# Kernel optimization log

Measured on AMD Instinct MI355X. Metric: run time of the kernel, lower is better.

The kernel has to match this reference:

```python
import jax, jax.numpy as jnp
import numpy as np

D_MODEL = 1024
N_HEADS = 16
D_HEAD = D_MODEL // N_HEADS
D_FF = 4096
EPS = 1e-5


def layer_norm(x, g, b):
    mu = jnp.mean(x, axis=-1, keepdims=True)
    var = jnp.mean(jnp.square(x - mu), axis=-1, keepdims=True)
    return (x - mu) * jax.lax.rsqrt(var + EPS) * g + b


def setup_inputs() -> dict:
    key = jax.random.key(0)
    ks = jax.random.split(key, 8)
    s = 1.0 / np.sqrt(D_MODEL)
    return {
        "x": jax.random.normal(ks[0], (2, 2048, D_MODEL), dtype=jnp.float32),
        "Wq": jax.random.normal(ks[1], (N_HEADS, D_MODEL, D_HEAD), dtype=jnp.float32) * s,
        "Wk": jax.random.normal(ks[2], (N_HEADS, D_MODEL, D_HEAD), dtype=jnp.float32) * s,
        "Wv": jax.random.normal(ks[3], (N_HEADS, D_MODEL, D_HEAD), dtype=jnp.float32) * s,
        "Wo": jax.random.normal(ks[4], (D_MODEL, D_MODEL), dtype=jnp.float32) * s,
        "bo": jnp.zeros((D_MODEL,), dtype=jnp.float32),
        "ln1_g": jnp.ones((D_MODEL,), dtype=jnp.float32),
        "ln1_b": jnp.zeros((D_MODEL,), dtype=jnp.float32),
        "ln2_g": jnp.ones((D_MODEL,), dtype=jnp.float32),
        "ln2_b": jnp.zeros((D_MODEL,), dtype=jnp.float32),
        "W1": jax.random.normal(ks[5], (D_MODEL, D_FF), dtype=jnp.float32) * s,
        "b1": jnp.zeros((D_FF,), dtype=jnp.float32),
        "W2": jax.random.normal(ks[6], (D_FF, D_MODEL), dtype=jnp.float32) * (1.0 / np.sqrt(D_FF)),
        "b2": jnp.zeros((D_MODEL,), dtype=jnp.float32),
    }


def reference(x, Wq, Wk, Wv, Wo, bo, ln1_g, ln1_b, ln2_g, ln2_b, W1, b1, W2, b2):
    # Pre-norm MHA (per-head projections batched over head axis h)
    xn = layer_norm(x, ln1_g, ln1_b)
    q = jnp.einsum("bsd,hde->bhse", xn, Wq)
    k = jnp.einsum("bsd,hde->bhse", xn, Wk)
    v = jnp.einsum("bsd,hde->bhse", xn, Wv)
    scores = jnp.einsum("bhqe,bhke->bhqk", q, k) / jnp.sqrt(jnp.float32(D_HEAD))
    w = jax.nn.softmax(scores, axis=-1)
    attn = jnp.einsum("bhqk,bhke->bhqe", w, v)  # [b,h,s,dh]
    b, h, s, dh = attn.shape
    concat = attn.transpose(0, 2, 1, 3).reshape(b, s, h * dh)  # head concat order matches torch cat
    attn_out = concat @ Wo + bo
    hidden = x + attn_out
    hn = layer_norm(hidden, ln2_g, ln2_b)
    ff = jax.nn.gelu(hn @ W1 + b1, approximate=False) @ W2 + b2  # torch nn.GELU default = exact
    return hidden + ff
```

## Files before the change

kernel.cpp:

```cpp
#include <hip/hip_runtime.h>
#include <hip/hip_bf16.h>

typedef __bf16 bf16;
typedef __bf16 bf16x4 __attribute__((ext_vector_type(4)));
typedef __bf16 bf16x8 __attribute__((ext_vector_type(8)));
typedef float  f32x4  __attribute__((ext_vector_type(4)));

static __device__ __forceinline__ f32x4 mfma16(bf16x8 a, bf16x8 b, f32x4 c) {
  return __builtin_amdgcn_mfma_f32_16x16x32_bf16(a, b, c, 0, 0, 0);
}

static __device__ __forceinline__ float fexp2(float x) {
  return __builtin_amdgcn_exp2f(x);
}

static __device__ __forceinline__ void gl_lds16(const bf16* g, bf16* l) {
  __builtin_amdgcn_global_load_lds(
      (const __attribute__((address_space(1))) void*)g,
      (__attribute__((address_space(3))) void*)l, 16, 0, 0);
}

struct TrTab {
  const float* src[6];
  bf16* dst[6];
  int R[6], C[6], ntx[6], nty[6];
  int base[7];
};

__global__ __launch_bounds__(256) void tr6_kernel(TrTab tab) {
  int bid = blockIdx.x;
  int j = 0;
  while (j < 5 && bid >= tab.base[j + 1]) ++j;
  const int local = bid - tab.base[j];
  const int R = tab.R[j], C = tab.C[j];
  const int ntx = tab.ntx[j];
  const int per_z = ntx * tab.nty[j];
  const int z = local / per_z;
  const int rem = local - z * per_z;
  const int by = rem / ntx, bx = rem - by * ntx;
  const float* in = tab.src[j];
  bf16* out = tab.dst[j];

  __shared__ bf16 tile[32][33];
  const size_t zoff = (size_t)z * R * C;
  const int tx = threadIdx.x & 31, ty = threadIdx.x >> 5;
  const int x = bx * 32 + tx;
  const int y0 = by * 32;
#pragma unroll
  for (int jj = 0; jj < 4; ++jj)
    tile[ty + jj * 8][tx] = (bf16)in[zoff + (size_t)(y0 + ty + jj * 8) * C + x];
  __syncthreads();
  const int x2 = y0 + tx;
  const int y2 = bx * 32;
#pragma unroll
  for (int jj = 0; jj < 4; ++jj)
    out[zoff + (size_t)(y2 + ty + jj * 8) * R + x2] = tile[tx][ty + jj * 8];
}

__global__ __launch_bounds__(256) void trb_kernel(const bf16* __restrict__ inp,
                                                  bf16* __restrict__ out,
                                                  int R, int C) {
  __shared__ bf16 tile[32][33];
  const size_t zoff = (size_t)blockIdx.z * R * C;
  const int tx = threadIdx.x & 31, ty = threadIdx.x >> 5;
  const int x = blockIdx.x * 32 + tx;
  const int y0 = blockIdx.y * 32;
#pragma unroll
  for (int j = 0; j < 4; ++j)
    tile[ty + j * 8][tx] = inp[zoff + (size_t)(y0 + ty + j * 8) * C + x];
  __syncthreads();
  const int x2 = y0 + tx;
  const int y2 = blockIdx.x * 32;
#pragma unroll
  for (int j = 0; j < 4; ++j)
    out[zoff + (size_t)(y2 + ty + j * 8) * R + x2] = tile[tx][ty + j * 8];
}

__global__ __launch_bounds__(256) void ln_kernel(const float* __restrict__ inp,
                                                 const float* __restrict__ g,
                                                 const float* __restrict__ bt,
                                                 bf16* __restrict__ outp) {
  const int row = blockIdx.x;
  const int t = threadIdx.x;
  f32x4 v = ((const f32x4*)inp)[row * 256 + t];
  float s = v[0] + v[1] + v[2] + v[3];
  float sq = v[0] * v[0] + v[1] * v[1] + v[2] * v[2] + v[3] * v[3];
#pragma unroll
  for (int off = 32; off > 0; off >>= 1) {
    s += __shfl_xor(s, off);
    sq += __shfl_xor(sq, off);
  }
  __shared__ float red[8];
  const int wave = t >> 6, lane = t & 63;
  if (lane == 0) {
    red[wave] = s;
    red[wave + 4] = sq;
  }
  __syncthreads();
  s = red[0] + red[1] + red[2] + red[3];
  sq = red[4] + red[5] + red[6] + red[7];
  const float mu = s * (1.0f / 1024.0f);
  const float var = sq * (1.0f / 1024.0f) - mu * mu;
  const float rstd = rsqrtf(fmaxf(var, 0.0f) + 1e-5f);
  f32x4 gg = ((const f32x4*)g)[t];
  f32x4 bb = ((const f32x4*)bt)[t];
  bf16 o[4];
#pragma unroll
  for (int i = 0; i < 4; ++i)
    o[i] = (bf16)((v[i] - mu) * rstd * gg[i] + bb[i]);
  *(uint2*)&outp[(size_t)row * 1024 + 4 * t] = *(uint2*)o;
}

enum { EPI_QKV = 0, EPI_O = 1, EPI_FF1 = 2, EPI_FF2 = 3 };

template <int EPI, bool NARROW>
__global__ __launch_bounds__(256) void gemm_bt(
    const bf16* __restrict__ A, const bf16* __restrict__ Bt, const int K,
    const float* __restrict__ bias, const float* __restrict__ res,
    bf16* __restrict__ outB, float* __restrict__ outF) {
  constexpr int BN = NARROW ? 64 : 128;
  constexpr int NI = NARROW ? 2 : 4;
  constexpr int BCH = BN / 32;
  __shared__ __align__(16) bf16 sA[2][128 * 64];
  __shared__ __align__(16) bf16 sB[2][BN * 64];
  const int t = threadIdx.x;
  const int lane = t & 63, wave = t >> 6;
  const int quad = lane >> 4, l15 = lane & 15;
  const int wr = wave >> 1, wc = wave & 1;

  const int gx = gridDim.x;
  const int nwg = gx * gridDim.y;
  const int lin = blockIdx.y * gx + blockIdx.x;
  const int sw = (lin & 7) * (nwg >> 3) + (lin >> 3);
  const int m0 = (sw / gx) * 128, n0 = (sw % gx) * BN;

  const int srow = lane >> 3;
  const int scol = ((lane & 7) ^ srow) * 8;

  const bf16* aPtr[4];
#pragma unroll
  for (int c = 0; c < 4; ++c)
    aPtr[c] = A + (size_t)(m0 + wave * 32 + c * 8 + srow) * K + scol;
  const bf16* bPtr[BCH];
#pragma unroll
  for (int c = 0; c < BCH; ++c)
    bPtr[c] = Bt + (size_t)(n0 + wave * (BCH * 8) + c * 8 + srow) * K + scol;

  f32x4 acc[4][NI];
#pragma unroll
  for (int i = 0; i < 4; ++i)
#pragma unroll
    for (int j = 0; j < NI; ++j) acc[i][j] = {0.f, 0.f, 0.f, 0.f};

  const int niter = K >> 6;
#pragma unroll
  for (int c = 0; c < 4; ++c)
    gl_lds16(aPtr[c], &sA[0][(wave * 4 + c) * 512]);
#pragma unroll
  for (int c = 0; c < BCH; ++c)
    gl_lds16(bPtr[c], &sB[0][(wave * BCH + c) * 512]);

  for (int it = 0; it < niter; ++it) {
    const int cur = it & 1, nxt = cur ^ 1;
    __syncthreads();
    if (it + 1 < niter) {
      const int off = (it + 1) * 64;
#pragma unroll
      for (int c = 0; c < 4; ++c)
        gl_lds16(aPtr[c] + off, &sA[nxt][(wave * 4 + c) * 512]);
#pragma unroll
      for (int c = 0; c < BCH; ++c)
        gl_lds16(bPtr[c] + off, &sB[nxt][(wave * BCH + c) * 512]);
    }
#pragma unroll
    for (int ks = 0; ks < 2; ++ks) {
      bf16x8 af[4], bfr[NI];
#pragma unroll
      for (int mi = 0; mi < 4; ++mi) {
        const int row = wr * 64 + mi * 16 + l15;
        const int col = ((ks * 4 + quad) ^ (row & 7)) * 8;
        af[mi] = *(const bf16x8*)&sA[cur][row * 64 + col];
      }
#pragma unroll
      for (int ni = 0; ni < NI; ++ni) {
        const int row = wc * (BN / 2) + ni * 16 + l15;
        const int col = ((ks * 4 + quad) ^ (row & 7)) * 8;
        bfr[ni] = *(const bf16x8*)&sB[cur][row * 64 + col];
      }
#pragma unroll
      for (int mi = 0; mi < 4; ++mi)
#pragma unroll
        for (int ni = 0; ni < NI; ++ni)
          acc[mi][ni] = mfma16(af[mi], bfr[ni], acc[mi][ni]);
    }
  }

#pragma unroll
  for (int mi = 0; mi < 4; ++mi) {
#pragma unroll
    for (int ni = 0; ni < NI; ++ni) {
      const int n = n0 + wc * (BN / 2) + ni * 16 + l15;
#pragma unroll
      for (int r = 0; r < 4; ++r) {
        const int m = m0 + wr * 64 + mi * 16 + quad * 4 + r;
        float v = acc[mi][ni][r];
        if constexpr (EPI == EPI_QKV) {
          const int which = n >> 10, nn = n & 1023;
          const int h = nn >> 6, e = nn & 63;
          const int b = m >> 11, s2 = m & 2047;
          outB[(size_t)which * 4194304 +
               ((size_t)(b * 16 + h) * 2048 + s2) * 64 + e] = (bf16)v;
        } else if constexpr (EPI == EPI_O) {
          v += bias[n] + res[(size_t)m * 1024 + n];
          outF[(size_t)m * 1024 + n] = v;
        } else if constexpr (EPI == EPI_FF1) {
          v += bias[n];
          v = 0.5f * v * (1.0f + erff(v * 0.70710678118654752f));
          outB[(size_t)m * 4096 + n] = (bf16)v;
        } else {
          v += bias[n] + res[(size_t)m * 1024 + n];
          outF[(size_t)m * 1024 + n] = v;
        }
      }
    }
  }
}

__global__ __launch_bounds__(512, 4) void attn_kernel(
    const bf16* __restrict__ q, const bf16* __restrict__ k,
    const bf16* __restrict__ vt, bf16* __restrict__ ao) {
  __shared__ __align__(16) bf16 sP[256 * 72];
  __shared__ __align__(16) bf16 sK[2][64 * 64];
  __shared__ __align__(16) bf16 sV[2][64 * 64];
  const int t = threadIdx.x;
  const int lane = t & 63, wave = t >> 6;
  const int wq = wave & 3, kh = wave >> 2;
  const int quad = lane >> 4, l15 = lane & 15;

  const int lin = blockIdx.y * 16 + blockIdx.x;
  const int sw = (lin & 7) * 64 + (lin >> 3);
  const int q0 = (sw & 15) * 128;
  const int bh = sw >> 4, b = bh >> 4, h = bh & 15;

  const bf16* Q  = q  + (size_t)bh * 2048 * 64;
  const bf16* Kp = k  + (size_t)bh * 2048 * 64 + (size_t)kh * 1024 * 64;
  const bf16* Vt = vt + (size_t)bh * 64 * 2048 + kh * 1024;
  const int srow = lane >> 3;
  const int scol = ((lane & 7) ^ srow) * 8;
  const float SCL = 0.125f * 1.4426950408889634f;

#pragma unroll
  for (int c = 0; c < 2; ++c) {
    const int chunk = wave * 2 + c;
    const int row = chunk * 8 + srow;
    gl_lds16(&Q[(size_t)(q0 + row) * 64 + scol], &sP[chunk * 512]);
  }
  __syncthreads();
  bf16x8 qf[2][2];
#pragma unroll
  for (int mi = 0; mi < 2; ++mi)
#pragma unroll
    for (int ks = 0; ks < 2; ++ks) {
      const int row = wq * 32 + mi * 16 + l15;
      const int col = ((ks * 4 + quad) ^ (row & 7)) * 8;
      qf[mi][ks] = *(const bf16x8*)&sP[row * 64 + col];
    }
  __syncthreads();

  f32x4 o[2][4];
  float ls[2] = {0.f, 0.f};
#pragma unroll
  for (int mi = 0; mi < 2; ++mi)
#pragma unroll
    for (int ne = 0; ne < 4; ++ne) o[mi][ne] = {0.f, 0.f, 0.f, 0.f};

  for (int kb = 0; kb < 16; ++kb) {
    const int kbase = kb * 64;
    __syncthreads();
#pragma unroll
    for (int c = 0; c < 2; ++c) {
      const int chunk = wq * 2 + c;
      const int row = chunk * 8 + srow;
      gl_lds16(&Kp[(size_t)(kbase + row) * 64 + scol], &sK[kh][chunk * 512]);
      gl_lds16(&Vt[(size_t)row * 2048 + kbase + scol], &sV[kh][chunk * 512]);
    }
    __syncthreads();

    f32x4 s[4][2];
#pragma unroll
    for (int ni = 0; ni < 4; ++ni)
#pragma unroll
      for (int mi = 0; mi < 2; ++mi) s[ni][mi] = {0.f, 0.f, 0.f, 0.f};
#pragma unroll
    for (int ks = 0; ks < 2; ++ks) {
      bf16x8 kf[4];
#pragma unroll
      for (int ni = 0; ni < 4; ++ni) {
        const int row = ni * 16 + l15;
        const int col = ((ks * 4 + quad) ^ (row & 7)) * 8;
        kf[ni] = *(const bf16x8*)&sK[kh][row * 64 + col];
      }
#pragma unroll
      for (int ni = 0; ni < 4; ++ni)
#pragma unroll
        for (int mi = 0; mi < 2; ++mi)
          s[ni][mi] = mfma16(kf[ni], qf[mi][ks], s[ni][mi]);
    }

#pragma unroll
    for (int mi = 0; mi < 2; ++mi)
#pragma unroll
      for (int ni = 0; ni < 4; ++ni) {
        bf16x4 p4;
#pragma unroll
        for (int r = 0; r < 4; ++r) {
          const float p = fexp2(s[ni][mi][r] * SCL);
          ls[mi] += p;
          p4[r] = (bf16)p;
        }
        *(bf16x4*)&sP[(wave * 32 + mi * 16 + l15) * 72 + ni * 16 + quad * 4] =
            p4;
      }

#pragma unroll
    for (int ksb = 0; ksb < 2; ++ksb) {
      bf16x8 vf[4];
#pragma unroll
      for (int ne = 0; ne < 4; ++ne) {
        const int row = ne * 16 + l15;
        const int col = ((ksb * 4 + quad) ^ (row & 7)) * 8;
        vf[ne] = *(const bf16x8*)&sV[kh][row * 64 + col];
      }
#pragma unroll
      for (int mi = 0; mi < 2; ++mi) {
        const bf16x8 pf = *(const bf16x8*)&sP[(wave * 32 + mi * 16 + l15) * 72 +
                                              ksb * 32 + quad * 8];
#pragma unroll
        for (int ne = 0; ne < 4; ++ne)
          o[mi][ne] = mfma16(pf, vf[ne], o[mi][ne]);
      }
    }
  }

#pragma unroll
  for (int mi = 0; mi < 2; ++mi) {
    ls[mi] += __shfl_xor(ls[mi], 16);
    ls[mi] += __shfl_xor(ls[mi], 32);
  }

  float* mo = (float*)sP;
  float* ml = (float*)sK;
  __syncthreads();
  if (kh == 1) {
    const int base = (wq * 64 + lane) * 32;
#pragma unroll
    for (int mi = 0; mi < 2; ++mi)
#pragma unroll
      for (int ne = 0; ne < 4; ++ne)
        *(f32x4*)&mo[base + (mi * 4 + ne) * 4] = o[mi][ne];
    ml[(wq * 64 + lane) * 2 + 0] = ls[0];
    ml[(wq * 64 + lane) * 2 + 1] = ls[1];
  }
  __syncthreads();
  if (kh == 0) {
    const int base = (wq * 64 + lane) * 32;
#pragma unroll
    for (int mi = 0; mi < 2; ++mi) {
#pragma unroll
      for (int ne = 0; ne < 4; ++ne) {
        const f32x4 add = *(const f32x4*)&mo[base + (mi * 4 + ne) * 4];
#pragma unroll
        for (int r = 0; r < 4; ++r) o[mi][ne][r] += add[r];
      }
      ls[mi] += ml[(wq * 64 + lane) * 2 + mi];
      ls[mi] = 1.0f / fmaxf(ls[mi], 1e-30f);
    }
#pragma unroll
    for (int mi = 0; mi < 2; ++mi) {
      float linv[4];
#pragma unroll
      for (int r = 0; r < 4; ++r) linv[r] = __shfl(ls[mi], quad * 4 + r);
#pragma unroll
      for (int ne = 0; ne < 4; ++ne)
#pragma unroll
        for (int r = 0; r < 4; ++r) {
          const int row = q0 + wq * 32 + mi * 16 + quad * 4 + r;
          const int col = h * 64 + ne * 16 + l15;
          ao[((size_t)(b * 2048 + row)) * 1024 + col] =
              (bf16)(o[mi][ne][r] * linv[r]);
        }
    }
  }
}

extern "C" void kernel_launch(void* const* d_in, const int* in_sizes, int n_in,
                              void* d_out, int out_size, void* d_ws,
                              size_t ws_size, hipStream_t stream) {
  const float* x    = (const float*)d_in[0];
  const float* Wq   = (const float*)d_in[1];
  const float* Wk   = (const float*)d_in[2];
  const float* Wv   = (const float*)d_in[3];
  const float* Wo   = (const float*)d_in[4];
  const float* bo   = (const float*)d_in[5];
  const float* ln1g = (const float*)d_in[6];
  const float* ln1b = (const float*)d_in[7];
  const float* ln2g = (const float*)d_in[8];
  const float* ln2b = (const float*)d_in[9];
  const float* W1   = (const float*)d_in[10];
  const float* b1   = (const float*)d_in[11];
  const float* W2   = (const float*)d_in[12];
  const float* b2   = (const float*)d_in[13];

  char* ws = (char*)d_ws;
  const size_t MB = 1ull << 20;
  bf16* QKVT = (bf16*)(ws);
  bf16* WqT  = QKVT;
  bf16* WkT  = (bf16*)(ws + 2 * MB);
  bf16* WvT  = (bf16*)(ws + 4 * MB);
  bf16* WoT  = (bf16*)(ws + 6 * MB);
  bf16* W1T  = (bf16*)(ws + 8 * MB);
  bf16* W2T  = (bf16*)(ws + 16 * MB);
  bf16* sh8  = (bf16*)(ws + 24 * MB);
  bf16* qb   = (bf16*)(ws + 32 * MB);
  bf16* kb   = (bf16*)(ws + 40 * MB);
  bf16* vb   = (bf16*)(ws + 48 * MB);
  bf16* vtb  = (bf16*)(ws + 56 * MB);
  bf16* h1   = (bf16*)(ws + 32 * MB);
  float* hid = (float*)(ws + 64 * MB);

  const dim3 blk(256);

  TrTab tab;
  const float* srcs[6] = {Wq, Wk, Wv, Wo, W1, W2};
  bf16* dsts[6] = {WqT, WkT, WvT, WoT, W1T, W2T};
  const int Rs[6] = {1024, 1024, 1024, 1024, 1024, 4096};
  const int Cs[6] = {64, 64, 64, 1024, 4096, 1024};
  const int Zs[6] = {16, 16, 16, 1, 1, 1};
  int base = 0;
  for (int j = 0; j < 6; ++j) {
    tab.src[j] = srcs[j];
    tab.dst[j] = dsts[j];
    tab.R[j] = Rs[j];
    tab.C[j] = Cs[j];
    tab.ntx[j] = Cs[j] / 32;
    tab.nty[j] = Rs[j] / 32;
    tab.base[j] = base;
    base += (Cs[j] / 32) * (Rs[j] / 32) * Zs[j];
  }
  tab.base[6] = base;
  tr6_kernel<<<base, blk, 0, stream>>>(tab);

  ln_kernel<<<4096, blk, 0, stream>>>(x, ln1g, ln1b, sh8);
  gemm_bt<EPI_QKV, false><<<dim3(24, 32), blk, 0, stream>>>(
      sh8, QKVT, 1024, nullptr, nullptr, qb, nullptr);
  trb_kernel<<<dim3(2, 64, 32), blk, 0, stream>>>(vb, vtb, 2048, 64);
  attn_kernel<<<dim3(16, 32), dim3(512), 0, stream>>>(qb, kb, vtb, sh8);
  gemm_bt<EPI_O, false><<<dim3(8, 32), blk, 0, stream>>>(
      sh8, WoT, 1024, bo, x, nullptr, hid);
  ln_kernel<<<4096, blk, 0, stream>>>(hid, ln2g, ln2b, sh8);
  gemm_bt<EPI_FF1, false><<<dim3(32, 32), blk, 0, stream>>>(
      sh8, W1T, 1024, b1, nullptr, h1, nullptr);
  gemm_bt<EPI_FF2, true><<<dim3(16, 32), blk, 0, stream>>>(
      h1, W2T, 4096, b2, hid, nullptr, (float*)d_out);

  (void)in_sizes; (void)n_in; (void)out_size; (void)ws_size;
}
```

Measured before the change: 357.3 us.

## Single-buffer GEMM LDS tiles and add XCD-aware block remap for FF2

Removes double buffering of the A/B LDS tiles in the GEMM: each iteration now issues its global-to-LDS loads, synchronizes, computes, then synchronizes again, halving LDS use per block. This can raise occupancy, but loads no longer overlap with MFMA work from the previous tile. It also replaces the old block-index swizzle with an optional XCD-grouped row mapping, enabled only for the FF2 GEMM. The other GEMMs now use plain blockIdx ordering with no swizzle.

Measured after the change: 368.1 us. 3.0% more time.

```diff
diff --git a/kernel.cpp b/kernel.cpp
--- a/kernel.cpp
+++ b/kernel.cpp
@@ -113,7 +113,7 @@
 
 enum { EPI_QKV = 0, EPI_O = 1, EPI_FF1 = 2, EPI_FF2 = 3 };
 
-template <int EPI, bool NARROW>
+template <int EPI, bool NARROW, bool SWZ>
 __global__ __launch_bounds__(256) void gemm_bt(
     const bf16* __restrict__ A, const bf16* __restrict__ Bt, const int K,
     const float* __restrict__ bias, const float* __restrict__ res,
@@ -121,18 +121,25 @@
   constexpr int BN = NARROW ? 64 : 128;
   constexpr int NI = NARROW ? 2 : 4;
   constexpr int BCH = BN / 32;
-  __shared__ __align__(16) bf16 sA[2][128 * 64];
-  __shared__ __align__(16) bf16 sB[2][BN * 64];
+  __shared__ __align__(16) bf16 sA[128 * 64];
+  __shared__ __align__(16) bf16 sB[BN * 64];
   const int t = threadIdx.x;
   const int lane = t & 63, wave = t >> 6;
   const int quad = lane >> 4, l15 = lane & 15;
   const int wr = wave >> 1, wc = wave & 1;
 
-  const int gx = gridDim.x;
-  const int nwg = gx * gridDim.y;
-  const int lin = blockIdx.y * gx + blockIdx.x;
-  const int sw = (lin & 7) * (nwg >> 3) + (lin >> 3);
-  const int m0 = (sw / gx) * 128, n0 = (sw % gx) * BN;
+  int bx, by;
+  if constexpr (SWZ) {
+    const int gy8 = gridDim.y >> 3;
+    const int lin = blockIdx.y * gridDim.x + blockIdx.x;
+    const int xcd = lin & 7, idx = lin >> 3;
+    by = xcd + 8 * (idx % gy8);
+    bx = idx / gy8;
+  } else {
+    bx = blockIdx.x;
+    by = blockIdx.y;
+  }
+  const int m0 = by * 128, n0 = bx * BN;
 
   const int srow = lane >> 3;
   const int scol = ((lane & 7) ^ srow) * 8;
@@ -153,25 +160,15 @@
     for (int j = 0; j < NI; ++j) acc[i][j] = {0.f, 0.f, 0.f, 0.f};
 
   const int niter = K >> 6;
-#pragma unroll
-  for (int c = 0; c < 4; ++c)
-    gl_lds16(aPtr[c], &sA[0][(wave * 4 + c) * 512]);
-#pragma unroll
-  for (int c = 0; c < BCH; ++c)
-    gl_lds16(bPtr[c], &sB[0][(wave * BCH + c) * 512]);
-
   for (int it = 0; it < niter; ++it) {
-    const int cur = it & 1, nxt = cur ^ 1;
+    const int off = it * 64;
+#pragma unroll
+    for (int c = 0; c < 4; ++c)
+      gl_lds16(aPtr[c] + off, &sA[(wave * 4 + c) * 512]);
+#pragma unroll
+    for (int c = 0; c < BCH; ++c)
+      gl_lds16(bPtr[c] + off, &sB[(wave * BCH + c) * 512]);
     __syncthreads();
-    if (it + 1 < niter) {
-      const int off = (it + 1) * 64;
-#pragma unroll
-      for (int c = 0; c < 4; ++c)
-        gl_lds16(aPtr[c] + off, &sA[nxt][(wave * 4 + c) * 512]);
-#pragma unroll
-      for (int c = 0; c < BCH; ++c)
-        gl_lds16(bPtr[c] + off, &sB[nxt][(wave * BCH + c) * 512]);
-    }
 #pragma unroll
     for (int ks = 0; ks < 2; ++ks) {
       bf16x8 af[4], bfr[NI];
@@ -179,13 +176,13 @@
       for (int mi = 0; mi < 4; ++mi) {
         const int row = wr * 64 + mi * 16 + l15;
         const int col = ((ks * 4 + quad) ^ (row & 7)) * 8;
-        af[mi] = *(const bf16x8*)&sA[cur][row * 64 + col];
+        af[mi] = *(const bf16x8*)&sA[row * 64 + col];
       }
 #pragma unroll
       for (int ni = 0; ni < NI; ++ni) {
         const int row = wc * (BN / 2) + ni * 16 + l15;
         const int col = ((ks * 4 + quad) ^ (row & 7)) * 8;
-        bfr[ni] = *(const bf16x8*)&sB[cur][row * 64 + col];
+        bfr[ni] = *(const bf16x8*)&sB[row * 64 + col];
       }
 #pragma unroll
       for (int mi = 0; mi < 4; ++mi)
@@ -193,6 +190,7 @@
         for (int ni = 0; ni < NI; ++ni)
           acc[mi][ni] = mfma16(af[mi], bfr[ni], acc[mi][ni]);
     }
+    __syncthreads();
   }
 
 #pragma unroll
@@ -451,16 +449,16 @@
   tr6_kernel<<<base, blk, 0, stream>>>(tab);
 
   ln_kernel<<<4096, blk, 0, stream>>>(x, ln1g, ln1b, sh8);
-  gemm_bt<EPI_QKV, false><<<dim3(24, 32), blk, 0, stream>>>(
+  gemm_bt<EPI_QKV, false, false><<<dim3(24, 32), blk, 0, stream>>>(
       sh8, QKVT, 1024, nullptr, nullptr, qb, nullptr);
   trb_kernel<<<dim3(2, 64, 32), blk, 0, stream>>>(vb, vtb, 2048, 64);
   attn_kernel<<<dim3(16, 32), dim3(512), 0, stream>>>(qb, kb, vtb, sh8);
-  gemm_bt<EPI_O, false><<<dim3(8, 32), blk, 0, stream>>>(
+  gemm_bt<EPI_O, false, false><<<dim3(8, 32), blk, 0, stream>>>(
       sh8, WoT, 1024, bo, x, nullptr, hid);
   ln_kernel<<<4096, blk, 0, stream>>>(hid, ln2g, ln2b, sh8);
-  gemm_bt<EPI_FF1, false><<<dim3(32, 32), blk, 0, stream>>>(
+  gemm_bt<EPI_FF1, false, false><<<dim3(32, 32), blk, 0, stream>>>(
       sh8, W1T, 1024, b1, nullptr, h1, nullptr);
-  gemm_bt<EPI_FF2, true><<<dim3(16, 32), blk, 0, stream>>>(
+  gemm_bt<EPI_FF2, true, true><<<dim3(16, 32), blk, 0, stream>>>(
       h1, W2T, 4096, b2, hid, nullptr, (float*)d_out);
 
   (void)in_sizes; (void)n_in; (void)out_size; (void)ws_size;
```
